# Performance work log

Hardware: AMD Instinct MI355X
Metric: run time of the kernel (lower is better)

## Reference

```python
import jax, jax.numpy as jnp
import numpy as np

V, E, H, C = 32320, 1024, 1024, 1024
T_DEC, T_CTX, B = 32, 32, 128


def setup_inputs() -> dict:
    key = jax.random.key(0)
    ks = jax.random.split(key, 10)
    s = 0.05
    tokens = jax.random.randint(ks[0], (T_DEC, B), 0, V)
    context = jax.random.normal(ks[1], (T_CTX, B, C), jnp.float32)
    ctx_len = jax.random.randint(ks[2], (B,), 1, T_CTX + 1)
    emb_table = jax.random.normal(ks[3], (V, E), jnp.float32) * s
    emb_table = emb_table.at[0].set(0.0)  # padding_idx=0
    W_ih = jax.random.normal(ks[4], (4 * H, E), jnp.float32) * s
    W_hh = jax.random.normal(ks[5], (4 * H, H), jnp.float32) * s
    b_ih = jnp.zeros((4 * H,), jnp.float32)
    b_hh = jnp.zeros((4 * H,), jnp.float32)
    Wq = jax.random.normal(ks[6], (H, H), jnp.float32) * s
    Wk = jax.random.normal(ks[7], (H, C), jnp.float32) * s
    v_att = jax.random.normal(ks[8], (H,), jnp.float32) * s
    att_bias = jnp.zeros((H,), jnp.float32)  # normalize_bias of BahdanauAttention
    norm_scalar = jnp.asarray(np.sqrt(1.0 / H), jnp.float32)
    return dict(ctx_len=ctx_len, tokens=tokens, context=context, emb_table=emb_table,
                W_ih=W_ih, W_hh=W_hh, b_ih=b_ih, b_hh=b_hh, Wq=Wq, Wk=Wk,
                v_att=v_att, att_bias=att_bias, norm_scalar=norm_scalar)


def reference(ctx_len, tokens, context, emb_table, W_ih, W_hh, b_ih, b_hh,
              Wq, Wk, v_att, att_bias, norm_scalar):
    # Embedding lookup (padding row 0 is zero in the table)
    emb = emb_table[tokens]                                   # (T_dec, B, E)
    Tq, Bsz = tokens.shape
    Hd = W_hh.shape[1]
    # --- LSTM (1 layer, h0 = c0 = 0), PyTorch gate order i,f,g,o ---
    xp = jnp.einsum('tbe,ge->tbg', emb, W_ih) + (b_ih + b_hh)  # (T,B,4H)

    def step(carry, x):
        h, c = carry
        g = x + h @ W_hh.T
        i, f, gg, o = jnp.split(g, 4, axis=-1)
        c = jax.nn.sigmoid(f) * c + jax.nn.sigmoid(i) * jnp.tanh(gg)
        h = jax.nn.sigmoid(o) * jnp.tanh(c)
        return (h, c), h

    h0 = jnp.zeros((Bsz, Hd), emb.dtype)
    _, rnn_out = jax.lax.scan(step, (h0, h0), xp)             # (T_dec, B, H)
    # --- normalized Bahdanau attention (batch_first internally) ---
    q = jnp.einsum('tbh,uh->btu', rnn_out, Wq)                # (B, Tq, U)
    k = jnp.einsum('tbc,uc->btu', context, Wk)                # (B, Tk, U)
    vn = norm_scalar * v_att / jnp.linalg.norm(v_att)
    scores = jnp.einsum('bqku,u->bqk',
                        jnp.tanh(q[:, :, None, :] + k[:, None, :, :] + att_bias), vn)
    Tk = context.shape[0]
    mask = jnp.arange(Tk)[None, :] >= ctx_len[:, None]        # (B, Tk) True = pad
    scores = jnp.where(mask[:, None, :], jnp.float32(-65504.0), scores)
    attn = jax.nn.softmax(scores, axis=-1)                    # (B, Tq, Tk)
    attn_out = jnp.einsum('bqk,kbc->qbc', attn, context)      # (Tq, B, C)
    # Stage5 returns (out7[2], out8) = (attn_outputs, rnn_outputs)
    return attn_out, rnn_out
```

## Files before the change

### kernel.cpp

```cpp
#include <hip/hip_runtime.h>
#include <hip/hip_bf16.h>
#include <math.h>

#define TDEC  32
#define TCTX  32
#define BATCH 128
#define HSZ   1024
#define ESZ   1024
#define CSZ   1024
#define G4    4096
#define MROWS 4096

typedef __attribute__((ext_vector_type(8))) __bf16 bf16x8;
typedef __attribute__((ext_vector_type(4))) float  f32x4;

__device__ __forceinline__ float sigmoidf_(float x) {
    return 1.0f / (1.0f + __expf(-x));
}
__device__ __forceinline__ float tanhf_(float x) {
    x = fminf(fmaxf(x, -15.0f), 15.0f);
    float e = __expf(2.0f * x);
    return (e - 1.0f) / (e + 1.0f);
}
__device__ __forceinline__ unsigned short f2bf(float x) {
    unsigned int u = __float_as_uint(x);
    unsigned int r = (u + 0x7FFFu + ((u >> 16) & 1u)) >> 16;
    return (unsigned short)r;
}
__device__ __forceinline__ float bf2f(unsigned short h) {
    return __uint_as_float(((unsigned int)h) << 16);
}
__device__ __forceinline__ uint4 pack8(float4 a, float4 b) {
    uint4 r;
    r.x = (unsigned)f2bf(a.x) | ((unsigned)f2bf(a.y) << 16);
    r.y = (unsigned)f2bf(a.z) | ((unsigned)f2bf(a.w) << 16);
    r.z = (unsigned)f2bf(b.x) | ((unsigned)f2bf(b.y) << 16);
    r.w = (unsigned)f2bf(b.z) | ((unsigned)f2bf(b.w) << 16);
    return r;
}

template <bool AGF, bool OUTB>
__launch_bounds__(256)
__global__ void gemm_bf16(const void* __restrict__ Ap,
                          const unsigned short* __restrict__ Bw,
                          const float* __restrict__ bias1, const float* __restrict__ bias2,
                          const int* __restrict__ gather, void* __restrict__ Cout,
                          int M, int N, int K)
{
    __shared__ __align__(16) unsigned short As[128 * 32];
    __shared__ __align__(16) unsigned short Bs[128 * 32];

    const int tid  = threadIdx.x;
    const int lane = tid & 63;
    const int w    = tid >> 6;
    const int m0   = blockIdx.y * 128;
    const int n0   = blockIdx.x * 128;
    const int srow = tid >> 2;
    const int slot = tid & 3;

    const unsigned short* pB0 = Bw + (size_t)(n0 + srow) * K + slot * 8;
    const unsigned short* pB1 = Bw + (size_t)(n0 + srow + 64) * K + slot * 8;

    const float* pAf0 = nullptr; const float* pAf1 = nullptr;
    const unsigned short* pAb0 = nullptr; const unsigned short* pAb1 = nullptr;
    if constexpr (AGF) {
        const float* Af = (const float*)Ap;
        const int r0 = gather[m0 + srow];
        const int r1 = gather[m0 + srow + 64];
        pAf0 = Af + (size_t)r0 * K + slot * 8;
        pAf1 = Af + (size_t)r1 * K + slot * 8;
    } else {
        const unsigned short* Ab = (const unsigned short*)Ap;
        pAb0 = Ab + (size_t)(m0 + srow) * K + slot * 8;
        pAb1 = Ab + (size_t)(m0 + srow + 64) * K + slot * 8;
    }

    uint4* dA0 = (uint4*)&As[srow * 32 + slot * 8];
    uint4* dA1 = (uint4*)&As[(srow + 64) * 32 + slot * 8];
    uint4* dB0 = (uint4*)&Bs[srow * 32 + slot * 8];
    uint4* dB1 = (uint4*)&Bs[(srow + 64) * 32 + slot * 8];

    const int fr = lane & 15;
    const int fk = (lane >> 4) * 8;
    const int wm = (w >> 1) * 64;
    const int wn = (w & 1) * 64;

    f32x4 acc[4][4];
    const f32x4 zero4 = {0.f, 0.f, 0.f, 0.f};
#pragma unroll
    for (int i = 0; i < 4; i++)
#pragma unroll
        for (int j = 0; j < 4; j++) acc[i][j] = zero4;

    uint4 rA0, rA1, rB0, rB1;
    float4 fA00, fA01, fA10, fA11;

    if constexpr (AGF) {
        fA00 = *(const float4*)(pAf0);  fA01 = *(const float4*)(pAf0 + 4);
        fA10 = *(const float4*)(pAf1);  fA11 = *(const float4*)(pAf1 + 4);
    } else {
        rA0 = *(const uint4*)(pAb0);    rA1 = *(const uint4*)(pAb1);
    }
    rB0 = *(const uint4*)(pB0);  rB1 = *(const uint4*)(pB1);

    for (int k0 = 0; k0 < K; k0 += 32) {
        if constexpr (AGF) { *dA0 = pack8(fA00, fA01); *dA1 = pack8(fA10, fA11); }
        else               { *dA0 = rA0;               *dA1 = rA1; }
        *dB0 = rB0; *dB1 = rB1;
        __syncthreads();

        const int kn = k0 + 32;
        if (kn < K) {
            if constexpr (AGF) {
                fA00 = *(const float4*)(pAf0 + kn);  fA01 = *(const float4*)(pAf0 + kn + 4);
                fA10 = *(const float4*)(pAf1 + kn);  fA11 = *(const float4*)(pAf1 + kn + 4);
            } else {
                rA0 = *(const uint4*)(pAb0 + kn);    rA1 = *(const uint4*)(pAb1 + kn);
            }
            rB0 = *(const uint4*)(pB0 + kn);  rB1 = *(const uint4*)(pB1 + kn);
        }

        bf16x8 a[4], b[4];
#pragma unroll
        for (int i = 0; i < 4; i++) a[i] = *(const bf16x8*)&As[(wm + i * 16 + fr) * 32 + fk];
#pragma unroll
        for (int j = 0; j < 4; j++) b[j] = *(const bf16x8*)&Bs[(wn + j * 16 + fr) * 32 + fk];
#pragma unroll
        for (int i = 0; i < 4; i++)
#pragma unroll
            for (int j = 0; j < 4; j++)
                acc[i][j] = __builtin_amdgcn_mfma_f32_16x16x32_bf16(a[i], b[j], acc[i][j], 0, 0, 0);
        __syncthreads();
    }

    const int orow = (lane >> 4) * 4;
#pragma unroll
    for (int j = 0; j < 4; j++) {
        const int col = n0 + wn + j * 16 + fr;
        float badd = 0.f;
        if (bias1) badd += bias1[col];
        if (bias2) badd += bias2[col];
#pragma unroll
        for (int i = 0; i < 4; i++) {
#pragma unroll
            for (int r = 0; r < 4; r++) {
                const int row = m0 + wm + i * 16 + orow + r;
                const float v = acc[i][j][r] + badd;
                if constexpr (OUTB)
                    ((unsigned short*)Cout)[(size_t)row * N + col] = f2bf(v);
                else
                    ((float*)Cout)[(size_t)row * N + col] = v;
            }
        }
    }
}

__launch_bounds__(256)
__global__ void lstm_step(const unsigned short* __restrict__ hprev,
                          const unsigned short* __restrict__ Whh,
                          const float* __restrict__ xp_t,
                          float* __restrict__ c,
                          float* __restrict__ hf,
                          unsigned short* __restrict__ hb)
{
    __shared__ __align__(16) unsigned short As[64 * 32];
    __shared__ __align__(16) unsigned short Bs[128 * 32];
    __shared__ float Gs[4][64][32];

    const int tid  = threadIdx.x;
    const int lane = tid & 63;
    const int w    = tid >> 6;
    const int m0   = blockIdx.y * 64;
    const int j0   = blockIdx.x * 32;

    const int srow = tid >> 2, slot = tid & 3;
    const unsigned short* pA = hprev + (size_t)(m0 + srow) * HSZ + slot * 8;
    const int lr1 = srow + 64;
    const unsigned short* pB0 = Whh + (size_t)((srow >> 5) * HSZ + j0 + (srow & 31)) * HSZ + slot * 8;
    const unsigned short* pB1 = Whh + (size_t)((lr1 >> 5) * HSZ + j0 + (lr1 & 31)) * HSZ + slot * 8;

    uint4* dA  = (uint4*)&As[srow * 32 + slot * 8];
    uint4* dB0 = (uint4*)&Bs[srow * 32 + slot * 8];
    uint4* dB1 = (uint4*)&Bs[lr1 * 32 + slot * 8];

    const int fr = lane & 15, fk = (lane >> 4) * 8;

    f32x4 acc[4][2];
    const f32x4 zero4 = {0.f, 0.f, 0.f, 0.f};
#pragma unroll
    for (int i = 0; i < 4; i++) { acc[i][0] = zero4; acc[i][1] = zero4; }

    uint4 rA = *(const uint4*)pA;
    uint4 rB0 = *(const uint4*)pB0;
    uint4 rB1 = *(const uint4*)pB1;

    for (int k0 = 0; k0 < HSZ; k0 += 32) {
        *dA = rA; *dB0 = rB0; *dB1 = rB1;
        __syncthreads();
        const int kn = k0 + 32;
        if (kn < HSZ) {
            rA  = *(const uint4*)(pA + kn);
            rB0 = *(const uint4*)(pB0 + kn);
            rB1 = *(const uint4*)(pB1 + kn);
        }
        bf16x8 a[4], b[2];
#pragma unroll
        for (int i = 0; i < 4; i++) a[i] = *(const bf16x8*)&As[(i * 16 + fr) * 32 + fk];
#pragma unroll
        for (int j = 0; j < 2; j++) b[j] = *(const bf16x8*)&Bs[(w * 32 + j * 16 + fr) * 32 + fk];
#pragma unroll
        for (int i = 0; i < 4; i++)
#pragma unroll
            for (int j = 0; j < 2; j++)
                acc[i][j] = __builtin_amdgcn_mfma_f32_16x16x32_bf16(a[i], b[j], acc[i][j], 0, 0, 0);
        __syncthreads();
    }

    const int orow = (lane >> 4) * 4;
#pragma unroll
    for (int i = 0; i < 4; i++)
#pragma unroll
        for (int j = 0; j < 2; j++)
#pragma unroll
            for (int r = 0; r < 4; r++)
                Gs[w][i * 16 + orow + r][j * 16 + fr] = acc[i][j][r];
    __syncthreads();

#pragma unroll
    for (int u = 0; u < 8; u++) {
        const int idx = u * 256 + tid;
        const int row = idx >> 5, col = idx & 31;
        const int bi = m0 + row, hj = j0 + col;
        const float* xr = xp_t + (size_t)bi * G4 + hj;
        const float gi = Gs[0][row][col] + xr[0];
        const float gf = Gs[1][row][col] + xr[HSZ];
        const float gg = Gs[2][row][col] + xr[2 * HSZ];
        const float go = Gs[3][row][col] + xr[3 * HSZ];
        const size_t ci = (size_t)bi * HSZ + hj;
        const float cn = sigmoidf_(gf) * c[ci] + sigmoidf_(gi) * tanhf_(gg);
        c[ci] = cn;
        const float h = sigmoidf_(go) * tanhf_(cn);
        hf[ci] = h;
        hb[ci] = f2bf(h);
    }
}

__global__ void lstm0(const float* __restrict__ xp0, float* __restrict__ c,
                      float* __restrict__ hf, unsigned short* __restrict__ hb)
{
    const int id = blockIdx.x * 256 + threadIdx.x;
    const int b = id >> 7, j8 = (id & 127) * 8;
    const float* g = xp0 + (size_t)b * G4 + j8;
    float gi[8], gf[8], gg[8], go[8];
#pragma unroll
    for (int e = 0; e < 8; e++) {
        gi[e] = g[e];
        gf[e] = g[HSZ + e];
        gg[e] = g[2 * HSZ + e];
        go[e] = g[3 * HSZ + e];
    }
    (void)gf;
    const size_t base = (size_t)b * HSZ + j8;
#pragma unroll
    for (int e = 0; e < 8; e++) {
        const float cn = sigmoidf_(gi[e]) * tanhf_(gg[e]);
        c[base + e] = cn;
        const float h = sigmoidf_(go[e]) * tanhf_(cn);
        hf[base + e] = h;
        hb[base + e] = f2bf(h);
    }
}

__global__ void cvt_f32_bf16(const float* __restrict__ in, unsigned short* __restrict__ out, int n8)
{
    const int id = blockIdx.x * 256 + threadIdx.x;
    if (id >= n8) return;
    const float4 a = *(const float4*)(in + (size_t)id * 8);
    const float4 b = *(const float4*)(in + (size_t)id * 8 + 4);
    *(uint4*)(out + (size_t)id * 8) = pack8(a, b);
}

__global__ void prep_vn(const float* __restrict__ v, const float* __restrict__ ns,
                        float* __restrict__ vn)
{
    __shared__ float red[16];
    __shared__ float total;
    const int tid = threadIdx.x;
    const float x = v[tid];
    float s = x * x;
#pragma unroll
    for (int o = 32; o > 0; o >>= 1) s += __shfl_down(s, o, 64);
    if ((tid & 63) == 0) red[tid >> 6] = s;
    __syncthreads();
    if (tid == 0) {
        float t = 0.f;
#pragma unroll
        for (int i = 0; i < 16; i++) t += red[i];
        total = sqrtf(t);
    }
    __syncthreads();
    vn[tid] = ns[0] * x / total;
}

__launch_bounds__(256)
__global__ void attn_kernel(const unsigned short* __restrict__ Q,
                            const unsigned short* __restrict__ Km,
                            const float* __restrict__ vn, const float* __restrict__ abias,
                            const unsigned short* __restrict__ ctx,
                            const int* __restrict__ ctx_len, float* __restrict__ out)
{
    const int bid = blockIdx.x;
    const int b = bid >> 5, tq = bid & 31, tid = threadIdx.x;

    const ushort4 qu = *(const ushort4*)&Q[((size_t)tq * BATCH + b) * HSZ + tid * 4];
    const float4 bv = *(const float4*)&abias[tid * 4];
    const float4 vv = *(const float4*)&vn[tid * 4];
    const float q0 = bf2f(qu.x) + bv.x, q1 = bf2f(qu.y) + bv.y;
    const float q2 = bf2f(qu.z) + bv.z, q3 = bf2f(qu.w) + bv.w;

    __shared__ float sc[TCTX];
    __shared__ float wred[4];

    for (int tk = 0; tk < TCTX; tk++) {
        const ushort4 ku = *(const ushort4*)&Km[((size_t)tk * BATCH + b) * HSZ + tid * 4];
        float p = vv.x * tanhf_(q0 + bf2f(ku.x))
                + vv.y * tanhf_(q1 + bf2f(ku.y))
                + vv.z * tanhf_(q2 + bf2f(ku.z))
                + vv.w * tanhf_(q3 + bf2f(ku.w));
#pragma unroll
        for (int o = 32; o > 0; o >>= 1) p += __shfl_down(p, o, 64);
        if ((tid & 63) == 0) wred[tid >> 6] = p;
        __syncthreads();
        if (tid == 0) sc[tk] = wred[0] + wred[1] + wred[2] + wred[3];
        __syncthreads();
    }

    const int cl = ctx_len[b];
    if (tid < 32) {
        float s = sc[tid];
        if (tid >= cl) s = -65504.0f;
        float m = s;
#pragma unroll
        for (int o = 16; o > 0; o >>= 1) m = fmaxf(m, __shfl_xor(m, o, 32));
        const float e = __expf(s - m);
        float d = e;
#pragma unroll
        for (int o = 16; o > 0; o >>= 1) d += __shfl_xor(d, o, 32);
        sc[tid] = e / d;
    }
    __syncthreads();

    float4 acc = {0.f, 0.f, 0.f, 0.f};
    for (int tk = 0; tk < TCTX; tk++) {
        const float wgt = sc[tk];
        const ushort4 cu = *(const ushort4*)&ctx[((size_t)tk * BATCH + b) * CSZ + tid * 4];
        acc.x = fmaf(wgt, bf2f(cu.x), acc.x);
        acc.y = fmaf(wgt, bf2f(cu.y), acc.y);
        acc.z = fmaf(wgt, bf2f(cu.z), acc.z);
        acc.w = fmaf(wgt, bf2f(cu.w), acc.w);
    }
    *reinterpret_cast<float4*>(&out[((size_t)tq * BATCH + b) * CSZ + tid * 4]) = acc;
}

extern "C" void kernel_launch(void* const* d_in, const int* in_sizes, int n_in,
                              void* d_out, int out_size, void* d_ws, size_t ws_size,
                              hipStream_t stream)
{
    const int*   ctx_len     = (const int*)d_in[0];
    const int*   tokens      = (const int*)d_in[1];
    const float* context     = (const float*)d_in[2];
    const float* emb_table   = (const float*)d_in[3];
    const float* W_ih        = (const float*)d_in[4];
    const float* W_hh        = (const float*)d_in[5];
    const float* b_ih        = (const float*)d_in[6];
    const float* b_hh        = (const float*)d_in[7];
    const float* Wq          = (const float*)d_in[8];
    const float* Wk          = (const float*)d_in[9];
    const float* v_att       = (const float*)d_in[10];
    const float* att_bias    = (const float*)d_in[11];
    const float* norm_scalar = (const float*)d_in[12];

    float* out      = (float*)d_out;
    float* attn_out = out;
    float* rnn_out  = out + (size_t)TDEC * BATCH * CSZ;

    char* W = (char*)d_ws;
    float*          xp     = (float*)W;
    unsigned short* q_bf   = (unsigned short*)W;
    unsigned short* k_bf   = (unsigned short*)(W + 8388608);
    unsigned short* Wq_bf  = (unsigned short*)(W + 16777216);
    unsigned short* Wk_bf  = (unsigned short*)(W + 18874368);
    unsigned short* Wih_bf = (unsigned short*)(W + 67108864);
    unsigned short* Whh_bf = (unsigned short*)(W + 75497472);
    unsigned short* ctx_bf = (unsigned short*)(W + 83886080);
    unsigned short* rnn_bf = (unsigned short*)(W + 92274688);
    float*          cst    = (float*)(W + 100663296);
    float*          vn     = (float*)(W + 101187584);

    prep_vn<<<1, 1024, 0, stream>>>(v_att, norm_scalar, vn);
    cvt_f32_bf16<<<2048, 256, 0, stream>>>(W_ih, Wih_bf, 524288);
    cvt_f32_bf16<<<2048, 256, 0, stream>>>(W_hh, Whh_bf, 524288);
    cvt_f32_bf16<<<2048, 256, 0, stream>>>(context, ctx_bf, 524288);

    gemm_bf16<true, false><<<dim3(32, 32), 256, 0, stream>>>(
        emb_table, Wih_bf, b_ih, b_hh, tokens, xp, MROWS, G4, ESZ);

    lstm0<<<64, 256, 0, stream>>>(xp, cst, rnn_out, rnn_bf);
    for (int t = 1; t < TDEC; t++) {
        lstm_step<<<dim3(32, 2), 256, 0, stream>>>(
            rnn_bf + (size_t)(t - 1) * BATCH * HSZ, Whh_bf,
            xp + (size_t)t * BATCH * G4, cst,
            rnn_out + (size_t)t * BATCH * HSZ,
            rnn_bf + (size_t)t * BATCH * HSZ);
    }

    cvt_f32_bf16<<<512, 256, 0, stream>>>(Wq, Wq_bf, 131072);
    cvt_f32_bf16<<<512, 256, 0, stream>>>(Wk, Wk_bf, 131072);
    gemm_bf16<false, true><<<dim3(8, 32), 256, 0, stream>>>(
        rnn_bf, Wq_bf, nullptr, nullptr, nullptr, q_bf, MROWS, HSZ, HSZ);
    gemm_bf16<false, true><<<dim3(8, 32), 256, 0, stream>>>(
        ctx_bf, Wk_bf, nullptr, nullptr, nullptr, k_bf, MROWS, HSZ, CSZ);

    attn_kernel<<<BATCH * TDEC, 256, 0, stream>>>(
        q_bf, k_bf, vn, att_bias, ctx_bf, ctx_len, attn_out);
}
```

Before: 974.6 us.

## Fuse LSTM steps into persistent cooperative kernel and batch attention queries per block

Replaces 32 per-timestep LSTM launches with a single cooperative kernel of 128 blocks. Each block holds its 32-row slice of W_hh in swizzled LDS for all steps, keeps the cell state in registers, and uses grid.sync between steps. This removes repeated launch overhead and repeated W_hh reloads from global memory. The attention kernel is also restructured: each block stages one batch's K into LDS and handles 8 queries, and uses a cheaper unclamped tanh. The cost is reliance on cooperative launch with all blocks co-resident, grid-wide barriers, and reading h_prev straight from global memory without LDS staging.

```diff
diff --git a/kernel.cpp b/kernel.cpp
--- a/kernel.cpp
+++ b/kernel.cpp
@@ -1,6 +1,9 @@
 #include <hip/hip_runtime.h>
 #include <hip/hip_bf16.h>
+#include <hip/hip_cooperative_groups.h>
 #include <math.h>
+
+namespace cg = cooperative_groups;
 
 #define TDEC  32
 #define TCTX  32
@@ -22,6 +25,10 @@
     float e = __expf(2.0f * x);
     return (e - 1.0f) / (e + 1.0f);
 }
+__device__ __forceinline__ float tanhfast(float x) {
+    float e = __expf(2.0f * x);
+    return 1.0f - 2.0f / (e + 1.0f);
+}
 __device__ __forceinline__ unsigned short f2bf(float x) {
     unsigned int u = __float_as_uint(x);
     unsigned int r = (u + 0x7FFFu + ((u >> 16) & 1u)) >> 16;
@@ -29,6 +36,12 @@
 }
 __device__ __forceinline__ float bf2f(unsigned short h) {
     return __uint_as_float(((unsigned int)h) << 16);
+}
+__device__ __forceinline__ float bf2f_lo(unsigned int v) {
+    return __uint_as_float(v << 16);
+}
+__device__ __forceinline__ float bf2f_hi(unsigned int v) {
+    return __uint_as_float(v & 0xFFFF0000u);
 }
 __device__ __forceinline__ uint4 pack8(float4 a, float4 b) {
     uint4 r;
@@ -156,118 +169,97 @@
 }
 
 __launch_bounds__(256)
-__global__ void lstm_step(const unsigned short* __restrict__ hprev,
-                          const unsigned short* __restrict__ Whh,
-                          const float* __restrict__ xp_t,
-                          float* __restrict__ c,
-                          float* __restrict__ hf,
-                          unsigned short* __restrict__ hb)
-{
-    __shared__ __align__(16) unsigned short As[64 * 32];
-    __shared__ __align__(16) unsigned short Bs[128 * 32];
-    __shared__ float Gs[4][64][32];
+__global__ void lstm_all(const unsigned short* __restrict__ Whh,
+                         const float* __restrict__ xp,
+                         float* __restrict__ rnn_out,
+                         unsigned short* __restrict__ rnn_bf)
+{
+    cg::grid_group grid = cg::this_grid();
+    __shared__ __align__(16) unsigned short Ws[32 * 1024];
+    __shared__ float Gs[128][33];
 
     const int tid  = threadIdx.x;
     const int lane = tid & 63;
     const int w    = tid >> 6;
-    const int m0   = blockIdx.y * 64;
-    const int j0   = blockIdx.x * 32;
-
-    const int srow = tid >> 2, slot = tid & 3;
-    const unsigned short* pA = hprev + (size_t)(m0 + srow) * HSZ + slot * 8;
-    const int lr1 = srow + 64;
-    const unsigned short* pB0 = Whh + (size_t)((srow >> 5) * HSZ + j0 + (srow & 31)) * HSZ + slot * 8;
-    const unsigned short* pB1 = Whh + (size_t)((lr1 >> 5) * HSZ + j0 + (lr1 & 31)) * HSZ + slot * 8;
-
-    uint4* dA  = (uint4*)&As[srow * 32 + slot * 8];
-    uint4* dB0 = (uint4*)&Bs[srow * 32 + slot * 8];
-    uint4* dB1 = (uint4*)&Bs[lr1 * 32 + slot * 8];
-
-    const int fr = lane & 15, fk = (lane >> 4) * 8;
-
-    f32x4 acc[4][2];
-    const f32x4 zero4 = {0.f, 0.f, 0.f, 0.f};
-#pragma unroll
-    for (int i = 0; i < 4; i++) { acc[i][0] = zero4; acc[i][1] = zero4; }
-
-    uint4 rA = *(const uint4*)pA;
-    uint4 rB0 = *(const uint4*)pB0;
-    uint4 rB1 = *(const uint4*)pB1;
-
-    for (int k0 = 0; k0 < HSZ; k0 += 32) {
-        *dA = rA; *dB0 = rB0; *dB1 = rB1;
-        __syncthreads();
-        const int kn = k0 + 32;
-        if (kn < HSZ) {
-            rA  = *(const uint4*)(pA + kn);
-            rB0 = *(const uint4*)(pB0 + kn);
-            rB1 = *(const uint4*)(pB1 + kn);
-        }
-        bf16x8 a[4], b[2];
-#pragma unroll
-        for (int i = 0; i < 4; i++) a[i] = *(const bf16x8*)&As[(i * 16 + fr) * 32 + fk];
-#pragma unroll
-        for (int j = 0; j < 2; j++) b[j] = *(const bf16x8*)&Bs[(w * 32 + j * 16 + fr) * 32 + fk];
-#pragma unroll
-        for (int i = 0; i < 4; i++)
-#pragma unroll
-            for (int j = 0; j < 2; j++)
-                acc[i][j] = __builtin_amdgcn_mfma_f32_16x16x32_bf16(a[i], b[j], acc[i][j], 0, 0, 0);
-        __syncthreads();
-    }
-
+    const int hj0  = blockIdx.x * 8;
+
+#pragma unroll
+    for (int i = 0; i < 16; i++) {
+        const int idx = i * 256 + tid;
+        const int n  = idx >> 7;
+        const int kb = idx & 127;
+        const int grow = (n >> 3) * HSZ + hj0 + (n & 7);
+        const uint4 v = *(const uint4*)(Whh + (size_t)grow * HSZ + kb * 8);
+        int byte = n * 2048 + kb * 16;
+        byte ^= (n & 7) << 4;
+        *(uint4*)((char*)Ws + byte) = v;
+    }
+    __syncthreads();
+
+    const int fr   = lane & 15;
+    const int fk   = (lane >> 4) * 8;
+    const int fkb  = fk * 2;
+    const int sw   = (fr & 7) << 4;
     const int orow = (lane >> 4) * 4;
-#pragma unroll
-    for (int i = 0; i < 4; i++)
-#pragma unroll
-        for (int j = 0; j < 2; j++)
-#pragma unroll
-            for (int r = 0; r < 4; r++)
-                Gs[w][i * 16 + orow + r][j * 16 + fr] = acc[i][j][r];
-    __syncthreads();
-
-#pragma unroll
-    for (int u = 0; u < 8; u++) {
-        const int idx = u * 256 + tid;
-        const int row = idx >> 5, col = idx & 31;
-        const int bi = m0 + row, hj = j0 + col;
-        const float* xr = xp_t + (size_t)bi * G4 + hj;
-        const float gi = Gs[0][row][col] + xr[0];
-        const float gf = Gs[1][row][col] + xr[HSZ];
-        const float gg = Gs[2][row][col] + xr[2 * HSZ];
-        const float go = Gs[3][row][col] + xr[3 * HSZ];
-        const size_t ci = (size_t)bi * HSZ + hj;
-        const float cn = sigmoidf_(gf) * c[ci] + sigmoidf_(gi) * tanhf_(gg);
-        c[ci] = cn;
-        const float h = sigmoidf_(go) * tanhf_(cn);
-        hf[ci] = h;
-        hb[ci] = f2bf(h);
-    }
-}
-
-__global__ void lstm0(const float* __restrict__ xp0, float* __restrict__ c,
-                      float* __restrict__ hf, unsigned short* __restrict__ hb)
-{
-    const int id = blockIdx.x * 256 + threadIdx.x;
-    const int b = id >> 7, j8 = (id & 127) * 8;
-    const float* g = xp0 + (size_t)b * G4 + j8;
-    float gi[8], gf[8], gg[8], go[8];
-#pragma unroll
-    for (int e = 0; e < 8; e++) {
-        gi[e] = g[e];
-        gf[e] = g[HSZ + e];
-        gg[e] = g[2 * HSZ + e];
-        go[e] = g[3 * HSZ + e];
-    }
-    (void)gf;
-    const size_t base = (size_t)b * HSZ + j8;
-#pragma unroll
-    for (int e = 0; e < 8; e++) {
-        const float cn = sigmoidf_(gi[e]) * tanhf_(gg[e]);
-        c[base + e] = cn;
-        const float h = sigmoidf_(go[e]) * tanhf_(cn);
-        hf[base + e] = h;
-        hb[base + e] = f2bf(h);
+    const char* wsb = (const char*)Ws;
+
+    float c_reg[4] = {0.f, 0.f, 0.f, 0.f};
+
+    for (int t = 0; t < TDEC; t++) {
+        if (t > 0) {
+            const unsigned short* hprev = rnn_bf + (size_t)(t - 1) * BATCH * HSZ;
+            const unsigned short* pa0 = hprev + (size_t)(32 * w + fr) * HSZ + fk;
+            const unsigned short* pa1 = hprev + (size_t)(32 * w + 16 + fr) * HSZ + fk;
+            f32x4 acc[2][2];
+            const f32x4 zero4 = {0.f, 0.f, 0.f, 0.f};
+            acc[0][0] = zero4; acc[0][1] = zero4; acc[1][0] = zero4; acc[1][1] = zero4;
+#pragma unroll 4
+            for (int k0 = 0; k0 < HSZ; k0 += 32) {
+                const bf16x8 a0 = *(const bf16x8*)(pa0 + k0);
+                const bf16x8 a1 = *(const bf16x8*)(pa1 + k0);
+                const int kbyte = k0 * 2 + fkb;
+                const bf16x8 b0 = *(const bf16x8*)(wsb + ((fr * 2048 + kbyte) ^ sw));
+                const bf16x8 b1 = *(const bf16x8*)(wsb + (((16 + fr) * 2048 + kbyte) ^ sw));
+                acc[0][0] = __builtin_amdgcn_mfma_f32_16x16x32_bf16(a0, b0, acc[0][0], 0, 0, 0);
+                acc[0][1] = __builtin_amdgcn_mfma_f32_16x16x32_bf16(a0, b1, acc[0][1], 0, 0, 0);
+                acc[1][0] = __builtin_amdgcn_mfma_f32_16x16x32_bf16(a1, b0, acc[1][0], 0, 0, 0);
+                acc[1][1] = __builtin_amdgcn_mfma_f32_16x16x32_bf16(a1, b1, acc[1][1], 0, 0, 0);
+            }
+#pragma unroll
+            for (int i = 0; i < 2; i++)
+#pragma unroll
+                for (int j = 0; j < 2; j++)
+#pragma unroll
+                    for (int r = 0; r < 4; r++)
+                        Gs[32 * w + i * 16 + orow + r][j * 16 + fr] = acc[i][j][r];
+            __syncthreads();
+        }
+
+        const float* xpt = xp + (size_t)t * BATCH * G4;
+#pragma unroll
+        for (int u = 0; u < 4; u++) {
+            const int idx = u * 256 + tid;
+            const int b  = idx >> 3;
+            const int jj = idx & 7;
+            const float* xr = xpt + (size_t)b * G4 + hj0 + jj;
+            float gi = xr[0];
+            float gf = xr[HSZ];
+            float gg = xr[2 * HSZ];
+            float go = xr[3 * HSZ];
+            if (t > 0) {
+                gi += Gs[b][jj];
+                gf += Gs[b][8 + jj];
+                gg += Gs[b][16 + jj];
+                go += Gs[b][24 + jj];
+            }
+            const float cn = sigmoidf_(gf) * c_reg[u] + sigmoidf_(gi) * tanhf_(gg);
+            c_reg[u] = cn;
+            const float h = sigmoidf_(go) * tanhf_(cn);
+            const size_t off = (size_t)t * BATCH * HSZ + (size_t)b * HSZ + hj0 + jj;
+            rnn_out[off] = h;
+            rnn_bf[off] = f2bf(h);
+        }
+        grid.sync();
     }
 }
 
@@ -309,57 +301,121 @@
                             const unsigned short* __restrict__ ctx,
                             const int* __restrict__ ctx_len, float* __restrict__ out)
 {
-    const int bid = blockIdx.x;
-    const int b = bid >> 5, tq = bid & 31, tid = threadIdx.x;
-
-    const ushort4 qu = *(const ushort4*)&Q[((size_t)tq * BATCH + b) * HSZ + tid * 4];
-    const float4 bv = *(const float4*)&abias[tid * 4];
-    const float4 vv = *(const float4*)&vn[tid * 4];
-    const float q0 = bf2f(qu.x) + bv.x, q1 = bf2f(qu.y) + bv.y;
-    const float q2 = bf2f(qu.z) + bv.z, q3 = bf2f(qu.w) + bv.w;
-
+    __shared__ __align__(16) unsigned short Ks[TCTX * HSZ];
     __shared__ float sc[TCTX];
-    __shared__ float wred[4];
-
-    for (int tk = 0; tk < TCTX; tk++) {
-        const ushort4 ku = *(const ushort4*)&Km[((size_t)tk * BATCH + b) * HSZ + tid * 4];
-        float p = vv.x * tanhf_(q0 + bf2f(ku.x))
-                + vv.y * tanhf_(q1 + bf2f(ku.y))
-                + vv.z * tanhf_(q2 + bf2f(ku.z))
-                + vv.w * tanhf_(q3 + bf2f(ku.w));
-#pragma unroll
-        for (int o = 32; o > 0; o >>= 1) p += __shfl_down(p, o, 64);
-        if ((tid & 63) == 0) wred[tid >> 6] = p;
+
+    const int blk = blockIdx.x;
+    const int b   = blk >> 2;
+    const int tq0 = (blk & 3) * 8;
+    const int tid = threadIdx.x;
+    const int lane = tid & 63;
+    const int w    = tid >> 6;
+
+#pragma unroll
+    for (int i = 0; i < 16; i++) {
+        const int idx = i * 256 + tid;
+        const int tk = idx >> 7, kb = idx & 127;
+        const uint4 v = *(const uint4*)(Km + ((size_t)tk * BATCH + b) * HSZ + kb * 8);
+        *(uint4*)((char*)Ks + tk * 2048 + kb * 16) = v;
+    }
+
+    float vnf[16], bsf[16];
+    {
+        const int u0 = 8 * lane, u1 = 512 + 8 * lane;
+        const float4 v0 = *(const float4*)(vn + u0);
+        const float4 v1 = *(const float4*)(vn + u0 + 4);
+        const float4 v2 = *(const float4*)(vn + u1);
+        const float4 v3 = *(const float4*)(vn + u1 + 4);
+        vnf[0]=v0.x; vnf[1]=v0.y; vnf[2]=v0.z; vnf[3]=v0.w;
+        vnf[4]=v1.x; vnf[5]=v1.y; vnf[6]=v1.z; vnf[7]=v1.w;
+        vnf[8]=v2.x; vnf[9]=v2.y; vnf[10]=v2.z; vnf[11]=v2.w;
+        vnf[12]=v3.x; vnf[13]=v3.y; vnf[14]=v3.z; vnf[15]=v3.w;
+        const float4 b0 = *(const float4*)(abias + u0);
+        const float4 b1 = *(const float4*)(abias + u0 + 4);
+        const float4 b2 = *(const float4*)(abias + u1);
+        const float4 b3 = *(const float4*)(abias + u1 + 4);
+        bsf[0]=b0.x; bsf[1]=b0.y; bsf[2]=b0.z; bsf[3]=b0.w;
+        bsf[4]=b1.x; bsf[5]=b1.y; bsf[6]=b1.z; bsf[7]=b1.w;
+        bsf[8]=b2.x; bsf[9]=b2.y; bsf[10]=b2.z; bsf[11]=b2.w;
+        bsf[12]=b3.x; bsf[13]=b3.y; bsf[14]=b3.z; bsf[15]=b3.w;
+    }
+    __syncthreads();
+
+    const int cl = ctx_len[b];
+
+    for (int q8 = 0; q8 < 8; q8++) {
+        const int tq = tq0 + q8;
+        const size_t qrow = ((size_t)tq * BATCH + b) * HSZ;
+        float qf[16];
+        {
+            const uint4 qa = *(const uint4*)(Q + qrow + 8 * lane);
+            const uint4 qb = *(const uint4*)(Q + qrow + 512 + 8 * lane);
+            qf[0]=bf2f_lo(qa.x)+bsf[0];  qf[1]=bf2f_hi(qa.x)+bsf[1];
+            qf[2]=bf2f_lo(qa.y)+bsf[2];  qf[3]=bf2f_hi(qa.y)+bsf[3];
+            qf[4]=bf2f_lo(qa.z)+bsf[4];  qf[5]=bf2f_hi(qa.z)+bsf[5];
+            qf[6]=bf2f_lo(qa.w)+bsf[6];  qf[7]=bf2f_hi(qa.w)+bsf[7];
+            qf[8]=bf2f_lo(qb.x)+bsf[8];  qf[9]=bf2f_hi(qb.x)+bsf[9];
+            qf[10]=bf2f_lo(qb.y)+bsf[10]; qf[11]=bf2f_hi(qb.y)+bsf[11];
+            qf[12]=bf2f_lo(qb.z)+bsf[12]; qf[13]=bf2f_hi(qb.z)+bsf[13];
+            qf[14]=bf2f_lo(qb.w)+bsf[14]; qf[15]=bf2f_hi(qb.w)+bsf[15];
+        }
+
+#pragma unroll
+        for (int i = 0; i < 8; i++) {
+            const int tk = w * 8 + i;
+            const uint4 ka = *(const uint4*)((const char*)Ks + tk * 2048 + lane * 16);
+            const uint4 kb = *(const uint4*)((const char*)Ks + tk * 2048 + 1024 + lane * 16);
+            float p;
+            p  = vnf[0]  * tanhfast(qf[0]  + bf2f_lo(ka.x));
+            p += vnf[1]  * tanhfast(qf[1]  + bf2f_hi(ka.x));
+            p += vnf[2]  * tanhfast(qf[2]  + bf2f_lo(ka.y));
+            p += vnf[3]  * tanhfast(qf[3]  + bf2f_hi(ka.y));
+            p += vnf[4]  * tanhfast(qf[4]  + bf2f_lo(ka.z));
+            p += vnf[5]  * tanhfast(qf[5]  + bf2f_hi(ka.z));
+            p += vnf[6]  * tanhfast(qf[6]  + bf2f_lo(ka.w));
+            p += vnf[7]  * tanhfast(qf[7]  + bf2f_hi(ka.w));
+            p += vnf[8]  * tanhfast(qf[8]  + bf2f_lo(kb.x));
+            p += vnf[9]  * tanhfast(qf[9]  + bf2f_hi(kb.x));
+            p += vnf[10] * tanhfast(qf[10] + bf2f_lo(kb.y));
+            p += vnf[11] * tanhfast(qf[11] + bf2f_hi(kb.y));
+            p += vnf[12] * tanhfast(qf[12] + bf2f_lo(kb.z));
+            p += vnf[13] * tanhfast(qf[13] + bf2f_hi(kb.z));
+            p += vnf[14] * tanhfast(qf[14] + bf2f_lo(kb.w));
+            p += vnf[15] * tanhfast(qf[15] + bf2f_hi(kb.w));
+#pragma unroll
+            for (int o = 32; o > 0; o >>= 1) p += __shfl_down(p, o, 64);
+            if (lane == 0) sc[tk] = p;
+        }
         __syncthreads();
-        if (tid == 0) sc[tk] = wred[0] + wred[1] + wred[2] + wred[3];
+
+        if (tid < 32) {
+            float s = sc[tid];
+            if (tid >= cl) s = -65504.0f;
+            float m = s;
+#pragma unroll
+            for (int o = 16; o > 0; o >>= 1) m = fmaxf(m, __shfl_xor(m, o, 32));
+            const float e = __expf(s - m);
+            float d = e;
+#pragma unroll
+            for (int o = 16; o > 0; o >>= 1) d += __shfl_xor(d, o, 32);
+            sc[tid] = e / d;
+        }
         __syncthreads();
-    }
-
-    const int cl = ctx_len[b];
-    if (tid < 32) {
-        float s = sc[tid];
-        if (tid >= cl) s = -65504.0f;
-        float m = s;
-#pragma unroll
-        for (int o = 16; o > 0; o >>= 1) m = fmaxf(m, __shfl_xor(m, o, 32));
-        const float e = __expf(s - m);
-        float d = e;
-#pragma unroll
-        for (int o = 16; o > 0; o >>= 1) d += __shfl_xor(d, o, 32);
-        sc[tid] = e / d;
-    }
-    __syncthreads();
-
-    float4 acc = {0.f, 0.f, 0.f, 0.f};
-    for (int tk = 0; tk < TCTX; tk++) {
-        const float wgt = sc[tk];
-        const ushort4 cu = *(const ushort4*)&ctx[((size_t)tk * BATCH + b) * CSZ + tid * 4];
-        acc.x = fmaf(wgt, bf2f(cu.x), acc.x);
-        acc.y = fmaf(wgt, bf2f(cu.y), acc.y);
-        acc.z = fmaf(wgt, bf2f(cu.z), acc.z);
-        acc.w = fmaf(wgt, bf2f(cu.w), acc.w);
-    }
-    *reinterpret_cast<float4*>(&out[((size_t)tq * BATCH + b) * CSZ + tid * 4]) = acc;
+
+        float4 acc = {0.f, 0.f, 0.f, 0.f};
+        const unsigned short* cb = ctx + (size_t)b * HSZ + tid * 4;
+#pragma unroll 4
+        for (int tk = 0; tk < TCTX; tk++) {
+            const float wgt = sc[tk];
+            const ushort4 cu = *(const ushort4*)(cb + (size_t)tk * BATCH * HSZ);
+            acc.x = fmaf(wgt, bf2f(cu.x), acc.x);
+            acc.y = fmaf(wgt, bf2f(cu.y), acc.y);
+            acc.z = fmaf(wgt, bf2f(cu.z), acc.z);
+            acc.w = fmaf(wgt, bf2f(cu.w), acc.w);
+        }
+        *(float4*)(out + qrow + tid * 4) = acc;
+        __syncthreads();
+    }
 }
 
 extern "C" void kernel_launch(void* const* d_in, const int* in_sizes, int n_in,
@@ -394,7 +450,6 @@
     unsigned short* Whh_bf = (unsigned short*)(W + 75497472);
     unsigned short* ctx_bf = (unsigned short*)(W + 83886080);
     unsigned short* rnn_bf = (unsigned short*)(W + 92274688);
-    float*          cst    = (float*)(W + 100663296);
     float*          vn     = (float*)(W + 101187584);
 
     prep_vn<<<1, 1024, 0, stream>>>(v_att, norm_scalar, vn);
@@ -405,13 +460,13 @@
     gemm_bf16<true, false><<<dim3(32, 32), 256, 0, stream>>>(
         emb_table, Wih_bf, b_ih, b_hh, tokens, xp, MROWS, G4, ESZ);
 
-    lstm0<<<64, 256, 0, stream>>>(xp, cst, rnn_out, rnn_bf);
-    for (int t = 1; t < TDEC; t++) {
-        lstm_step<<<dim3(32, 2), 256, 0, stream>>>(
-            rnn_bf + (size_t)(t - 1) * BATCH * HSZ, Whh_bf,
-            xp + (size_t)t * BATCH * G4, cst,
-            rnn_out + (size_t)t * BATCH * HSZ,
-            rnn_bf + (size_t)t * BATCH * HSZ);
+    {
+        const unsigned short* whh_arg = Whh_bf;
+        const float* xp_arg = xp;
+        float* rnn_arg = rnn_out;
+        unsigned short* rnnbf_arg = rnn_bf;
+        void* args[] = {(void*)&whh_arg, (void*)&xp_arg, (void*)&rnn_arg, (void*)&rnnbf_arg};
+        hipLaunchCooperativeKernel((void*)lstm_all, dim3(128), dim3(256), args, 0, stream);
     }
 
     cvt_f32_bf16<<<512, 256, 0, stream>>>(Wq, Wq_bf, 131072);
@@ -421,6 +476,6 @@
     gemm_bf16<false, true><<<dim3(8, 32), 256, 0, stream>>>(
         ctx_bf, Wk_bf, nullptr, nullptr, nullptr, k_bf, MROWS, HSZ, CSZ);
 
-    attn_kernel<<<BATCH * TDEC, 256, 0, stream>>>(
+    attn_kernel<<<512, 256, 0, stream>>>(
         q_bf, k_bf, vn, att_bias, ctx_bf, ctx_len, attn_out);
 }
```

Result: slower. 1.440 ms (+47.8%).
